# Optimization experiments

Hardware: AMD Instinct MI355X
Metric: run time of the kernel (lower is better)

Reference implementation:

```python
import jax, jax.numpy as jnp
import numpy as np

B, N = 128, 128
FEAT_IN = 6   # feature_dim(4) + class + score
E = 32        # embedding_dim
NUM_CLASSES = 80


def setup_inputs() -> dict:
    key = jax.random.key(0)
    ks = jax.random.split(key, 20)
    def glorot(k, shape):
        fan_in, fan_out = shape[0], shape[1]
        lim = jnp.sqrt(6.0 / (fan_in + fan_out)).astype(jnp.float32)
        return jax.random.uniform(k, shape, jnp.float32, -lim, lim)
    return {
        'boxes': jax.random.uniform(ks[0], (B, N, 4), jnp.float32),
        'classes': jax.random.randint(ks[1], (B, N), 0, NUM_CLASSES),
        'scores': jax.random.uniform(ks[2], (B, N), jnp.float32),
        'num_objects': jax.random.randint(ks[3], (B,), 1, N + 1),
        # feature_encoder: Linear(6->32), ReLU, Linear(32->32)
        'W1': glorot(ks[4], (FEAT_IN, E)), 'b1': jnp.zeros((E,), jnp.float32),
        'W2': glorot(ks[5], (E, E)),       'b2': jnp.zeros((E,), jnp.float32),
        # isObject: Linear(32->32), ReLU, Linear(32->1), Sigmoid
        'Wo1': glorot(ks[6], (E, E)),  'bo1': jnp.zeros((E,), jnp.float32),
        'Wo2': glorot(ks[7], (E, 1)),  'bo2': jnp.zeros((1,), jnp.float32),
        # sameClass: Linear(64->32), ReLU, Linear(32->1), Sigmoid
        'Ws1': glorot(ks[8], (2 * E, E)), 'bs1': jnp.zeros((E,), jnp.float32),
        'Ws2': glorot(ks[9], (E, 1)),     'bs2': jnp.zeros((1,), jnp.float32),
    }


def reference(boxes, classes, scores, num_objects, W1, b1, W2, b2,
              Wo1, bo1, Wo2, bo2, Ws1, bs1, Ws2, bs2):
    # encode: [B,N,6] -> [B,N,E]
    combined = jnp.concatenate(
        [boxes, classes.astype(jnp.float32)[..., None], scores[..., None]], axis=-1)
    enc = jax.nn.relu(combined @ W1 + b1) @ W2 + b2                 # [B,N,E]

    # isObject predicate -> [B,N]
    isobj = jax.nn.sigmoid(jax.nn.relu(enc @ Wo1 + bo1) @ Wo2 + bo2)[..., 0]

    # sameClass on all pairs: split concat-weight so we never build [B,N,N,2E]
    Wsx, Wsy = Ws1[:E], Ws1[E:]
    hx = enc @ Wsx                                                  # [B,N,E]
    hy = enc @ Wsy                                                  # [B,N,E]
    h = jax.nn.relu(hx[:, :, None, :] + hy[:, None, :, :] + bs1)    # [B,N,N,E]
    same = jax.nn.sigmoid(h @ Ws2 + bs2)[..., 0]                    # [B,N,N] (x,y)

    # inner = And_min(isObject(y), sameClass(x,y))
    inner = jnp.minimum(isobj[:, None, :], same)                    # [B,N,N]

    mask = jnp.arange(N)[None, :] < num_objects[:, None]            # [B,N] valid objs
    n = num_objects.astype(jnp.float32)
    denom = jnp.maximum(n, 1.0)

    # Exists_y = mean over valid y
    exists = jnp.sum(inner * mask[:, None, :], axis=-1) / denom[:, None]  # [B,N]

    # outer = Or_max(Not(isObject(x)), exists)
    outer = jnp.maximum(1.0 - isobj, exists)                        # [B,N]

    # Forall_x = min over valid x (pad with 1.0, never the min for valid batches)
    sat_b = jnp.min(jnp.where(mask, outer, 1.0), axis=-1)           # [B]

    valid = (num_objects > 0).astype(jnp.float32)
    cnt = jnp.sum(valid)
    total = jnp.where(cnt > 0,
                      jnp.sum(sat_b * valid) / jnp.maximum(cnt, 1.0),
                      jnp.float32(1.0))
    return total
```

## Files before the change

kernel.cpp:

```cpp
#include <hip/hip_runtime.h>

#define BB 128
#define NN 128
#define EE 32

#define SAT_OFF 0
#define CNT_OFF 128
#define HX_OFF  256
#define HY_OFF  (HX_OFF + 16384 * 32)
#define ISO_OFF (HY_OFF + 16384 * 32)

__global__ __launch_bounds__(256) void encode_kernel(
    const float* __restrict__ boxes, const int* __restrict__ classes,
    const float* __restrict__ scores,
    const float* __restrict__ W1, const float* __restrict__ b1,
    const float* __restrict__ W2, const float* __restrict__ b2,
    const float* __restrict__ Wo1, const float* __restrict__ bo1,
    const float* __restrict__ Wo2, const float* __restrict__ bo2,
    const float* __restrict__ Ws1, float* __restrict__ ws)
{
    __shared__ float sm[4740];

    const int t = threadIdx.x;

    if (blockIdx.x == 0) {
        if (t < 128) ((unsigned*)ws)[SAT_OFF + t] = 0x7F7F7F7Fu;
        if (t == 128) ((unsigned*)ws)[CNT_OFF] = 0u;
    }

    ((float4*)(sm + 224))[t]        = ((const float4*)W2)[t];
    ((float4*)(sm + 1280))[t]       = ((const float4*)Wo1)[t];
    ((float4*)(sm + 2692))[t]       = ((const float4*)Ws1)[t];
    ((float4*)(sm + 2692))[t + 256] = ((const float4*)Ws1)[t + 256];
    if (t < 48) ((float4*)sm)[t] = ((const float4*)W1)[t];
    if (t < 32) {
        sm[192 + t]  = b1[t];
        sm[1248 + t] = b2[t];
        sm[2304 + t] = bo1[t];
        sm[2336 + t] = Wo2[t];
    }
    if (t == 0) sm[2368] = bo2[0];
    __syncthreads();

    const int il = t >> 5;
    const int e  = t & 31;
    const int item = blockIdx.x * 8 + il;

    const float4 bx = ((const float4*)boxes)[item];
    const float c4 = (float)classes[item];
    const float c5 = scores[item];

    float h1 = sm[192 + e];
    h1 = fmaf(bx.x, sm[0 * 32 + e], h1);
    h1 = fmaf(bx.y, sm[1 * 32 + e], h1);
    h1 = fmaf(bx.z, sm[2 * 32 + e], h1);
    h1 = fmaf(bx.w, sm[3 * 32 + e], h1);
    h1 = fmaf(c4,   sm[4 * 32 + e], h1);
    h1 = fmaf(c5,   sm[5 * 32 + e], h1);
    h1 = fmaxf(h1, 0.f);

    float* row = sm + 2372 + il * 40;
    row[e] = h1;

    float a0 = 0.f, a1 = 0.f, a2 = 0.f, a3 = 0.f;
#pragma unroll
    for (int kk = 0; kk < 8; kk++) {
        const float4 h = *(const float4*)(row + kk * 4);
        a0 = fmaf(h.x, sm[224 + (4 * kk + 0) * 32 + e], a0);
        a1 = fmaf(h.y, sm[224 + (4 * kk + 1) * 32 + e], a1);
        a2 = fmaf(h.z, sm[224 + (4 * kk + 2) * 32 + e], a2);
        a3 = fmaf(h.w, sm[224 + (4 * kk + 3) * 32 + e], a3);
    }
    const float enc = ((a0 + a1) + (a2 + a3)) + sm[1248 + e];
    row[e] = enc;

    float u = sm[2304 + e];
    float hx = 0.f, hy = 0.f;
#pragma unroll
    for (int kk = 0; kk < 8; kk++) {
        const float4 ec = *(const float4*)(row + kk * 4);
        const int k0 = 4 * kk;
        u  = fmaf(ec.x, sm[1280 + (k0 + 0) * 32 + e], u);
        u  = fmaf(ec.y, sm[1280 + (k0 + 1) * 32 + e], u);
        u  = fmaf(ec.z, sm[1280 + (k0 + 2) * 32 + e], u);
        u  = fmaf(ec.w, sm[1280 + (k0 + 3) * 32 + e], u);
        hx = fmaf(ec.x, sm[2692 + (k0 + 0) * 32 + e], hx);
        hx = fmaf(ec.y, sm[2692 + (k0 + 1) * 32 + e], hx);
        hx = fmaf(ec.z, sm[2692 + (k0 + 2) * 32 + e], hx);
        hx = fmaf(ec.w, sm[2692 + (k0 + 3) * 32 + e], hx);
        hy = fmaf(ec.x, sm[2692 + (32 + k0 + 0) * 32 + e], hy);
        hy = fmaf(ec.y, sm[2692 + (32 + k0 + 1) * 32 + e], hy);
        hy = fmaf(ec.z, sm[2692 + (32 + k0 + 2) * 32 + e], hy);
        hy = fmaf(ec.w, sm[2692 + (32 + k0 + 3) * 32 + e], hy);
    }
    u = fmaxf(u, 0.f);

    float v = u * sm[2336 + e];
    v += __shfl_xor(v, 16, 32);
    v += __shfl_xor(v, 8, 32);
    v += __shfl_xor(v, 4, 32);
    v += __shfl_xor(v, 2, 32);
    v += __shfl_xor(v, 1, 32);

    ws[HX_OFF + item * 32 + e] = hx;
    ws[HY_OFF + item * 32 + e] = hy;
    if (e == 0)
        ws[ISO_OFF + item] = 1.f / (1.f + __expf(-(v + sm[2368])));
}

__global__ __launch_bounds__(256) void pairs_kernel(
    const float* __restrict__ bs1, const float* __restrict__ Ws2,
    const float* __restrict__ bs2, const int* __restrict__ num_objects,
    float* __restrict__ ws, float* __restrict__ out, int nblocks)
{
    __shared__ float hyS[128 * 36];
    __shared__ float hxS[32 * 36];
    __shared__ float isoS[128];
    __shared__ float wred[4];
    __shared__ int lastFlag;
    __shared__ float r1[4], r2[4];

    const int t = threadIdx.x;
    const int b = blockIdx.x >> 2;
    const int q = blockIdx.x & 3;

    const float4* hyg4 = (const float4*)(ws + HY_OFF + b * 128 * 32);
#pragma unroll
    for (int it = 0; it < 4; it++) {
        const int idx = t + it * 256;
        ((float4*)(hyS + (idx >> 3) * 36))[idx & 7] = hyg4[idx];
    }
    {
        const float4* hxg4 = (const float4*)(ws + HX_OFF + (b * 128 + q * 32) * 32);
        ((float4*)(hxS + (t >> 3) * 36))[t & 7] = hxg4[t];
    }
    if (t < 128) isoS[t] = ws[ISO_OFF + b * 128 + t];
    __syncthreads();

    const int nb = num_objects[b];
    const int il = t >> 3;
    const int i  = q * 32 + il;
    const int s  = t & 7;

    float hxb[32];
#pragma unroll
    for (int kk = 0; kk < 8; kk++) {
        const float4 h = ((const float4*)(hxS + il * 36))[kk];
        hxb[4 * kk + 0] = h.x + bs1[4 * kk + 0];
        hxb[4 * kk + 1] = h.y + bs1[4 * kk + 1];
        hxb[4 * kk + 2] = h.z + bs1[4 * kk + 2];
        hxb[4 * kk + 3] = h.w + bs1[4 * kk + 3];
    }
    float w2[32];
#pragma unroll
    for (int k = 0; k < 32; k++) w2[k] = Ws2[k];
    const float bbias = bs2[0];

    float acc = 0.f;
    for (int j = s; j < nb; j += 8) {
        const float4* hr4 = (const float4*)(hyS + j * 36);
        float d0 = bbias, d1 = 0.f, d2 = 0.f, d3 = 0.f;
#pragma unroll
        for (int kk = 0; kk < 8; kk++) {
            const float4 h = hr4[kk];
            const int k0 = 4 * kk;
            d0 = fmaf(fmaxf(hxb[k0 + 0] + h.x, 0.f), w2[k0 + 0], d0);
            d1 = fmaf(fmaxf(hxb[k0 + 1] + h.y, 0.f), w2[k0 + 1], d1);
            d2 = fmaf(fmaxf(hxb[k0 + 2] + h.z, 0.f), w2[k0 + 2], d2);
            d3 = fmaf(fmaxf(hxb[k0 + 3] + h.w, 0.f), w2[k0 + 3], d3);
        }
        const float d = (d0 + d1) + (d2 + d3);
        const float same = 1.f / (1.f + __expf(-d));
        acc += fminf(isoS[j], same);
    }
    acc += __shfl_xor(acc, 1);
    acc += __shfl_xor(acc, 2);
    acc += __shfl_xor(acc, 4);

    const float exists = acc / (float)(nb > 1 ? nb : 1);
    const float outer = fmaxf(1.f - isoS[i], exists);
    float val = (i < nb) ? outer : 1.f;

    val = fminf(val, __shfl_xor(val, 8));
    val = fminf(val, __shfl_xor(val, 16));
    val = fminf(val, __shfl_xor(val, 32));
    if ((t & 63) == 0) wred[t >> 6] = val;
    __syncthreads();

    if (t == 0) {
        const float m = fminf(fminf(wred[0], wred[1]), fminf(wred[2], wred[3]));
        atomicMin((unsigned*)ws + SAT_OFF + b, __float_as_uint(m));
        __threadfence();
        const unsigned old = __hip_atomic_fetch_add((unsigned*)ws + CNT_OFF, 1u,
                                                    __ATOMIC_ACQ_REL, __HIP_MEMORY_SCOPE_AGENT);
        lastFlag = (old == (unsigned)(nblocks - 1)) ? 1 : 0;
    }
    __syncthreads();

    if (lastFlag) {
        float contrib = 0.f, vcnt = 0.f;
        if (t < 128) {
            const int nbt = num_objects[t];
            const unsigned sbits = __hip_atomic_load((unsigned*)ws + SAT_OFF + t,
                                                     __ATOMIC_RELAXED, __HIP_MEMORY_SCOPE_AGENT);
            const float sat = __uint_as_float(sbits);
            const float valid = (nbt > 0) ? 1.f : 0.f;
            contrib = sat * valid;
            vcnt = valid;
        }
#pragma unroll
        for (int off = 1; off < 64; off <<= 1) {
            contrib += __shfl_xor(contrib, off);
            vcnt += __shfl_xor(vcnt, off);
        }
        if ((t & 63) == 0) { r1[t >> 6] = contrib; r2[t >> 6] = vcnt; }
        __syncthreads();
        if (t == 0) {
            const float sc = r1[0] + r1[1] + r1[2] + r1[3];
            const float cn = r2[0] + r2[1] + r2[2] + r2[3];
            out[0] = (cn > 0.f) ? (sc / cn) : 1.f;
        }
    }
}

extern "C" void kernel_launch(void* const* d_in, const int* in_sizes, int n_in,
                              void* d_out, int out_size, void* d_ws, size_t ws_size,
                              hipStream_t stream)
{
    const float* boxes       = (const float*)d_in[0];
    const int*   classes     = (const int*)d_in[1];
    const float* scores      = (const float*)d_in[2];
    const int*   num_objects = (const int*)d_in[3];
    const float* W1  = (const float*)d_in[4];
    const float* b1  = (const float*)d_in[5];
    const float* W2  = (const float*)d_in[6];
    const float* b2  = (const float*)d_in[7];
    const float* Wo1 = (const float*)d_in[8];
    const float* bo1 = (const float*)d_in[9];
    const float* Wo2 = (const float*)d_in[10];
    const float* bo2 = (const float*)d_in[11];
    const float* Ws1 = (const float*)d_in[12];
    const float* bs1 = (const float*)d_in[13];
    const float* Ws2 = (const float*)d_in[14];
    const float* bs2 = (const float*)d_in[15];

    float* ws  = (float*)d_ws;
    float* out = (float*)d_out;

    encode_kernel<<<2048, 256, 0, stream>>>(boxes, classes, scores,
                                            W1, b1, W2, b2, Wo1, bo1, Wo2, bo2,
                                            Ws1, ws);
    const int nblocks = 128 * 4;
    pairs_kernel<<<nblocks, 256, 0, stream>>>(bs1, Ws2, bs2, num_objects,
                                              ws, out, nblocks);
}
```

Measured before the change: 112.0 us.

## Compute encoder MLP with one thread per object using register arrays

Restructures the encode kernel so each thread processes a whole object, keeping hidden, encoding, hx, hy and u vectors in registers. Weights are read directly from global memory with uniform indices (scalar loads), replacing the shared-memory staging, barrier and warp-shuffle reduction. The launch changes to 256 blocks of 64 threads. Outputs are written as float4 stores per item. The cost is heavy register pressure (about 128+ live floats), possible spills, and far fewer waves in flight to hide latency.

Result: slower. 159.5 us (+42.4%).

```diff
diff --git a/kernel.cpp b/kernel.cpp
--- a/kernel.cpp
+++ b/kernel.cpp
@@ -10,7 +10,7 @@
 #define HY_OFF  (HX_OFF + 16384 * 32)
 #define ISO_OFF (HY_OFF + 16384 * 32)
 
-__global__ __launch_bounds__(256) void encode_kernel(
+__global__ __launch_bounds__(64, 1) void encode_kernel(
     const float* __restrict__ boxes, const int* __restrict__ classes,
     const float* __restrict__ scores,
     const float* __restrict__ W1, const float* __restrict__ b1,
@@ -19,93 +19,70 @@
     const float* __restrict__ Wo2, const float* __restrict__ bo2,
     const float* __restrict__ Ws1, float* __restrict__ ws)
 {
-    __shared__ float sm[4740];
-
     const int t = threadIdx.x;
+    const int item = blockIdx.x * 64 + t;
 
     if (blockIdx.x == 0) {
-        if (t < 128) ((unsigned*)ws)[SAT_OFF + t] = 0x7F7F7F7Fu;
-        if (t == 128) ((unsigned*)ws)[CNT_OFF] = 0u;
-    }
-
-    ((float4*)(sm + 224))[t]        = ((const float4*)W2)[t];
-    ((float4*)(sm + 1280))[t]       = ((const float4*)Wo1)[t];
-    ((float4*)(sm + 2692))[t]       = ((const float4*)Ws1)[t];
-    ((float4*)(sm + 2692))[t + 256] = ((const float4*)Ws1)[t + 256];
-    if (t < 48) ((float4*)sm)[t] = ((const float4*)W1)[t];
-    if (t < 32) {
-        sm[192 + t]  = b1[t];
-        sm[1248 + t] = b2[t];
-        sm[2304 + t] = bo1[t];
-        sm[2336 + t] = Wo2[t];
-    }
-    if (t == 0) sm[2368] = bo2[0];
-    __syncthreads();
-
-    const int il = t >> 5;
-    const int e  = t & 31;
-    const int item = blockIdx.x * 8 + il;
+        ((unsigned*)ws)[SAT_OFF + t]      = 0x7F7F7F7Fu;
+        ((unsigned*)ws)[SAT_OFF + 64 + t] = 0x7F7F7F7Fu;
+        if (t == 0) ((unsigned*)ws)[CNT_OFF] = 0u;
+    }
 
     const float4 bx = ((const float4*)boxes)[item];
     const float c4 = (float)classes[item];
     const float c5 = scores[item];
 
-    float h1 = sm[192 + e];
-    h1 = fmaf(bx.x, sm[0 * 32 + e], h1);
-    h1 = fmaf(bx.y, sm[1 * 32 + e], h1);
-    h1 = fmaf(bx.z, sm[2 * 32 + e], h1);
-    h1 = fmaf(bx.w, sm[3 * 32 + e], h1);
-    h1 = fmaf(c4,   sm[4 * 32 + e], h1);
-    h1 = fmaf(c5,   sm[5 * 32 + e], h1);
-    h1 = fmaxf(h1, 0.f);
-
-    float* row = sm + 2372 + il * 40;
-    row[e] = h1;
-
-    float a0 = 0.f, a1 = 0.f, a2 = 0.f, a3 = 0.f;
+    float h[32];
+#pragma unroll
+    for (int e = 0; e < 32; e++) {
+        float v = b1[e];
+        v = fmaf(bx.x, W1[0 * 32 + e], v);
+        v = fmaf(bx.y, W1[1 * 32 + e], v);
+        v = fmaf(bx.z, W1[2 * 32 + e], v);
+        v = fmaf(bx.w, W1[3 * 32 + e], v);
+        v = fmaf(c4,   W1[4 * 32 + e], v);
+        v = fmaf(c5,   W1[5 * 32 + e], v);
+        h[e] = fmaxf(v, 0.f);
+    }
+
+    float enc[32];
+#pragma unroll
+    for (int e = 0; e < 32; e++) enc[e] = b2[e];
+#pragma unroll
+    for (int k = 0; k < 32; k++) {
+        const float hk = h[k];
+#pragma unroll
+        for (int e = 0; e < 32; e++)
+            enc[e] = fmaf(hk, W2[k * 32 + e], enc[e]);
+    }
+
+    float u[32], hx[32], hy[32];
+#pragma unroll
+    for (int e = 0; e < 32; e++) { u[e] = bo1[e]; hx[e] = 0.f; hy[e] = 0.f; }
+#pragma unroll
+    for (int k = 0; k < 32; k++) {
+        const float ek = enc[k];
+#pragma unroll
+        for (int e = 0; e < 32; e++) {
+            u[e]  = fmaf(ek, Wo1[k * 32 + e], u[e]);
+            hx[e] = fmaf(ek, Ws1[k * 32 + e], hx[e]);
+            hy[e] = fmaf(ek, Ws1[(32 + k) * 32 + e], hy[e]);
+        }
+    }
+
+    float z = bo2[0];
+#pragma unroll
+    for (int e = 0; e < 32; e++)
+        z = fmaf(fmaxf(u[e], 0.f), Wo2[e], z);
+
+    float4* ox = (float4*)(ws + HX_OFF + item * 32);
+    float4* oy = (float4*)(ws + HY_OFF + item * 32);
 #pragma unroll
     for (int kk = 0; kk < 8; kk++) {
-        const float4 h = *(const float4*)(row + kk * 4);
-        a0 = fmaf(h.x, sm[224 + (4 * kk + 0) * 32 + e], a0);
-        a1 = fmaf(h.y, sm[224 + (4 * kk + 1) * 32 + e], a1);
-        a2 = fmaf(h.z, sm[224 + (4 * kk + 2) * 32 + e], a2);
-        a3 = fmaf(h.w, sm[224 + (4 * kk + 3) * 32 + e], a3);
-    }
-    const float enc = ((a0 + a1) + (a2 + a3)) + sm[1248 + e];
-    row[e] = enc;
-
-    float u = sm[2304 + e];
-    float hx = 0.f, hy = 0.f;
-#pragma unroll
-    for (int kk = 0; kk < 8; kk++) {
-        const float4 ec = *(const float4*)(row + kk * 4);
-        const int k0 = 4 * kk;
-        u  = fmaf(ec.x, sm[1280 + (k0 + 0) * 32 + e], u);
-        u  = fmaf(ec.y, sm[1280 + (k0 + 1) * 32 + e], u);
-        u  = fmaf(ec.z, sm[1280 + (k0 + 2) * 32 + e], u);
-        u  = fmaf(ec.w, sm[1280 + (k0 + 3) * 32 + e], u);
-        hx = fmaf(ec.x, sm[2692 + (k0 + 0) * 32 + e], hx);
-        hx = fmaf(ec.y, sm[2692 + (k0 + 1) * 32 + e], hx);
-        hx = fmaf(ec.z, sm[2692 + (k0 + 2) * 32 + e], hx);
-        hx = fmaf(ec.w, sm[2692 + (k0 + 3) * 32 + e], hx);
-        hy = fmaf(ec.x, sm[2692 + (32 + k0 + 0) * 32 + e], hy);
-        hy = fmaf(ec.y, sm[2692 + (32 + k0 + 1) * 32 + e], hy);
-        hy = fmaf(ec.z, sm[2692 + (32 + k0 + 2) * 32 + e], hy);
-        hy = fmaf(ec.w, sm[2692 + (32 + k0 + 3) * 32 + e], hy);
-    }
-    u = fmaxf(u, 0.f);
-
-    float v = u * sm[2336 + e];
-    v += __shfl_xor(v, 16, 32);
-    v += __shfl_xor(v, 8, 32);
-    v += __shfl_xor(v, 4, 32);
-    v += __shfl_xor(v, 2, 32);
-    v += __shfl_xor(v, 1, 32);
-
-    ws[HX_OFF + item * 32 + e] = hx;
-    ws[HY_OFF + item * 32 + e] = hy;
-    if (e == 0)
-        ws[ISO_OFF + item] = 1.f / (1.f + __expf(-(v + sm[2368])));
+        ox[kk] = make_float4(hx[4 * kk], hx[4 * kk + 1], hx[4 * kk + 2], hx[4 * kk + 3]);
+        oy[kk] = make_float4(hy[4 * kk], hy[4 * kk + 1], hy[4 * kk + 2], hy[4 * kk + 3]);
+    }
+    ws[ISO_OFF + item] = 1.f / (1.f + __expf(-z));
 }
 
 __global__ __launch_bounds__(256) void pairs_kernel(
@@ -247,9 +224,9 @@
     float* ws  = (float*)d_ws;
     float* out = (float*)d_out;
 
-    encode_kernel<<<2048, 256, 0, stream>>>(boxes, classes, scores,
-                                            W1, b1, W2, b2, Wo1, bo1, Wo2, bo2,
-                                            Ws1, ws);
+    encode_kernel<<<256, 64, 0, stream>>>(boxes, classes, scores,
+                                          W1, b1, W2, b2, Wo1, bo1, Wo2, bo2,
+                                          Ws1, ws);
     const int nblocks = 128 * 4;
     pairs_kernel<<<nblocks, 256, 0, stream>>>(bs1, Ws2, bs2, num_objects,
                                               ws, out, nblocks);
```

## Keep encoder weights in registers and double per-thread work in pairs kernel

Applied to the files above, without the earlier changes.

The encode kernel no longer stages all weights into shared memory. Each thread instead keeps its weight column in registers and processes four items per warp-group, with a quarter as many blocks, so weight loads are amortized. The pairs kernel has each thread handle two x rows against each loaded hy row, which halves the block count and the hy reloads from shared memory per pair. The cost is much higher register pressure (over 130 floats in encode, 64+ in pairs), which can lower occupancy, and fewer blocks means less parallelism on a large GPU.

Measured after the change: 102.4 us. 1.09x faster.

```diff
diff --git a/kernel.cpp b/kernel.cpp
--- a/kernel.cpp
+++ b/kernel.cpp
@@ -19,93 +19,100 @@
     const float* __restrict__ Wo2, const float* __restrict__ bo2,
     const float* __restrict__ Ws1, float* __restrict__ ws)
 {
-    __shared__ float sm[4740];
+    __shared__ float rows[8 * 36];
 
     const int t = threadIdx.x;
+    const int e = t & 31;
+    const int g = t >> 5;
 
     if (blockIdx.x == 0) {
         if (t < 128) ((unsigned*)ws)[SAT_OFF + t] = 0x7F7F7F7Fu;
         if (t == 128) ((unsigned*)ws)[CNT_OFF] = 0u;
     }
 
-    ((float4*)(sm + 224))[t]        = ((const float4*)W2)[t];
-    ((float4*)(sm + 1280))[t]       = ((const float4*)Wo1)[t];
-    ((float4*)(sm + 2692))[t]       = ((const float4*)Ws1)[t];
-    ((float4*)(sm + 2692))[t + 256] = ((const float4*)Ws1)[t + 256];
-    if (t < 48) ((float4*)sm)[t] = ((const float4*)W1)[t];
-    if (t < 32) {
-        sm[192 + t]  = b1[t];
-        sm[1248 + t] = b2[t];
-        sm[2304 + t] = bo1[t];
-        sm[2336 + t] = Wo2[t];
-    }
-    if (t == 0) sm[2368] = bo2[0];
-    __syncthreads();
-
-    const int il = t >> 5;
-    const int e  = t & 31;
-    const int item = blockIdx.x * 8 + il;
-
-    const float4 bx = ((const float4*)boxes)[item];
-    const float c4 = (float)classes[item];
-    const float c5 = scores[item];
-
-    float h1 = sm[192 + e];
-    h1 = fmaf(bx.x, sm[0 * 32 + e], h1);
-    h1 = fmaf(bx.y, sm[1 * 32 + e], h1);
-    h1 = fmaf(bx.z, sm[2 * 32 + e], h1);
-    h1 = fmaf(bx.w, sm[3 * 32 + e], h1);
-    h1 = fmaf(c4,   sm[4 * 32 + e], h1);
-    h1 = fmaf(c5,   sm[5 * 32 + e], h1);
-    h1 = fmaxf(h1, 0.f);
-
-    float* row = sm + 2372 + il * 40;
-    row[e] = h1;
-
-    float a0 = 0.f, a1 = 0.f, a2 = 0.f, a3 = 0.f;
-#pragma unroll
-    for (int kk = 0; kk < 8; kk++) {
-        const float4 h = *(const float4*)(row + kk * 4);
-        a0 = fmaf(h.x, sm[224 + (4 * kk + 0) * 32 + e], a0);
-        a1 = fmaf(h.y, sm[224 + (4 * kk + 1) * 32 + e], a1);
-        a2 = fmaf(h.z, sm[224 + (4 * kk + 2) * 32 + e], a2);
-        a3 = fmaf(h.w, sm[224 + (4 * kk + 3) * 32 + e], a3);
-    }
-    const float enc = ((a0 + a1) + (a2 + a3)) + sm[1248 + e];
-    row[e] = enc;
-
-    float u = sm[2304 + e];
-    float hx = 0.f, hy = 0.f;
-#pragma unroll
-    for (int kk = 0; kk < 8; kk++) {
-        const float4 ec = *(const float4*)(row + kk * 4);
-        const int k0 = 4 * kk;
-        u  = fmaf(ec.x, sm[1280 + (k0 + 0) * 32 + e], u);
-        u  = fmaf(ec.y, sm[1280 + (k0 + 1) * 32 + e], u);
-        u  = fmaf(ec.z, sm[1280 + (k0 + 2) * 32 + e], u);
-        u  = fmaf(ec.w, sm[1280 + (k0 + 3) * 32 + e], u);
-        hx = fmaf(ec.x, sm[2692 + (k0 + 0) * 32 + e], hx);
-        hx = fmaf(ec.y, sm[2692 + (k0 + 1) * 32 + e], hx);
-        hx = fmaf(ec.z, sm[2692 + (k0 + 2) * 32 + e], hx);
-        hx = fmaf(ec.w, sm[2692 + (k0 + 3) * 32 + e], hx);
-        hy = fmaf(ec.x, sm[2692 + (32 + k0 + 0) * 32 + e], hy);
-        hy = fmaf(ec.y, sm[2692 + (32 + k0 + 1) * 32 + e], hy);
-        hy = fmaf(ec.z, sm[2692 + (32 + k0 + 2) * 32 + e], hy);
-        hy = fmaf(ec.w, sm[2692 + (32 + k0 + 3) * 32 + e], hy);
-    }
-    u = fmaxf(u, 0.f);
-
-    float v = u * sm[2336 + e];
-    v += __shfl_xor(v, 16, 32);
-    v += __shfl_xor(v, 8, 32);
-    v += __shfl_xor(v, 4, 32);
-    v += __shfl_xor(v, 2, 32);
-    v += __shfl_xor(v, 1, 32);
-
-    ws[HX_OFF + item * 32 + e] = hx;
-    ws[HY_OFF + item * 32 + e] = hy;
-    if (e == 0)
-        ws[ISO_OFF + item] = 1.f / (1.f + __expf(-(v + sm[2368])));
+    float w1c[6];
+#pragma unroll
+    for (int f = 0; f < 6; f++) w1c[f] = W1[f * 32 + e];
+    float w2c[32], wo1c[32], wsxc[32], wsyc[32];
+#pragma unroll
+    for (int k = 0; k < 32; k++) {
+        w2c[k]  = W2[k * 32 + e];
+        wo1c[k] = Wo1[k * 32 + e];
+        wsxc[k] = Ws1[k * 32 + e];
+        wsyc[k] = Ws1[(32 + k) * 32 + e];
+    }
+    const float b1e  = b1[e];
+    const float b2e  = b2[e];
+    const float bo1e = bo1[e];
+    const float wo2e = Wo2[e];
+    const float bo2s = bo2[0];
+
+    float* row = rows + g * 36;
+    const int itemBase = blockIdx.x * 32 + g * 4;
+
+#pragma unroll 1
+    for (int it = 0; it < 4; ++it) {
+        const int item = itemBase + it;
+
+        const float4 bx = ((const float4*)boxes)[item];
+        const float c4 = (float)classes[item];
+        const float c5 = scores[item];
+
+        float h1 = b1e;
+        h1 = fmaf(bx.x, w1c[0], h1);
+        h1 = fmaf(bx.y, w1c[1], h1);
+        h1 = fmaf(bx.z, w1c[2], h1);
+        h1 = fmaf(bx.w, w1c[3], h1);
+        h1 = fmaf(c4,   w1c[4], h1);
+        h1 = fmaf(c5,   w1c[5], h1);
+        h1 = fmaxf(h1, 0.f);
+
+        row[e] = h1;
+
+        float a0 = 0.f, a1 = 0.f, a2 = 0.f, a3 = 0.f;
+#pragma unroll
+        for (int kk = 0; kk < 8; kk++) {
+            const float4 h = *(const float4*)(row + kk * 4);
+            a0 = fmaf(h.x, w2c[4 * kk + 0], a0);
+            a1 = fmaf(h.y, w2c[4 * kk + 1], a1);
+            a2 = fmaf(h.z, w2c[4 * kk + 2], a2);
+            a3 = fmaf(h.w, w2c[4 * kk + 3], a3);
+        }
+        const float enc = ((a0 + a1) + (a2 + a3)) + b2e;
+        row[e] = enc;
+
+        float u = bo1e, hx = 0.f, hy = 0.f;
+#pragma unroll
+        for (int kk = 0; kk < 8; kk++) {
+            const float4 ec = *(const float4*)(row + kk * 4);
+            const int k0 = 4 * kk;
+            u  = fmaf(ec.x, wo1c[k0 + 0], u);
+            u  = fmaf(ec.y, wo1c[k0 + 1], u);
+            u  = fmaf(ec.z, wo1c[k0 + 2], u);
+            u  = fmaf(ec.w, wo1c[k0 + 3], u);
+            hx = fmaf(ec.x, wsxc[k0 + 0], hx);
+            hx = fmaf(ec.y, wsxc[k0 + 1], hx);
+            hx = fmaf(ec.z, wsxc[k0 + 2], hx);
+            hx = fmaf(ec.w, wsxc[k0 + 3], hx);
+            hy = fmaf(ec.x, wsyc[k0 + 0], hy);
+            hy = fmaf(ec.y, wsyc[k0 + 1], hy);
+            hy = fmaf(ec.z, wsyc[k0 + 2], hy);
+            hy = fmaf(ec.w, wsyc[k0 + 3], hy);
+        }
+        u = fmaxf(u, 0.f);
+
+        float v = u * wo2e;
+        v += __shfl_xor(v, 16, 32);
+        v += __shfl_xor(v, 8, 32);
+        v += __shfl_xor(v, 4, 32);
+        v += __shfl_xor(v, 2, 32);
+        v += __shfl_xor(v, 1, 32);
+
+        ws[HX_OFF + item * 32 + e] = hx;
+        ws[HY_OFF + item * 32 + e] = hy;
+        if (e == 0)
+            ws[ISO_OFF + item] = 1.f / (1.f + __expf(-(v + bo2s)));
+    }
 }
 
 __global__ __launch_bounds__(256) void pairs_kernel(
@@ -114,15 +121,15 @@
     float* __restrict__ ws, float* __restrict__ out, int nblocks)
 {
     __shared__ float hyS[128 * 36];
-    __shared__ float hxS[32 * 36];
+    __shared__ float hxS[64 * 36];
     __shared__ float isoS[128];
     __shared__ float wred[4];
     __shared__ int lastFlag;
     __shared__ float r1[4], r2[4];
 
     const int t = threadIdx.x;
-    const int b = blockIdx.x >> 2;
-    const int q = blockIdx.x & 3;
+    const int b = blockIdx.x >> 1;
+    const int half = blockIdx.x & 1;
 
     const float4* hyg4 = (const float4*)(ws + HY_OFF + b * 128 * 32);
 #pragma unroll
@@ -130,56 +137,73 @@
         const int idx = t + it * 256;
         ((float4*)(hyS + (idx >> 3) * 36))[idx & 7] = hyg4[idx];
     }
-    {
-        const float4* hxg4 = (const float4*)(ws + HX_OFF + (b * 128 + q * 32) * 32);
-        ((float4*)(hxS + (t >> 3) * 36))[t & 7] = hxg4[t];
+    const float4* hxg4 = (const float4*)(ws + HX_OFF + (b * 128 + half * 64) * 32);
+#pragma unroll
+    for (int it = 0; it < 2; it++) {
+        const int idx = t + it * 256;
+        ((float4*)(hxS + (idx >> 3) * 36))[idx & 7] = hxg4[idx];
     }
     if (t < 128) isoS[t] = ws[ISO_OFF + b * 128 + t];
     __syncthreads();
 
     const int nb = num_objects[b];
-    const int il = t >> 3;
-    const int i  = q * 32 + il;
+    const int p  = t >> 3;
+    const int i0 = half * 64 + p * 2;
+    const int i1 = i0 + 1;
     const int s  = t & 7;
 
-    float hxb[32];
+    float hxb0[32], hxb1[32];
 #pragma unroll
     for (int kk = 0; kk < 8; kk++) {
-        const float4 h = ((const float4*)(hxS + il * 36))[kk];
-        hxb[4 * kk + 0] = h.x + bs1[4 * kk + 0];
-        hxb[4 * kk + 1] = h.y + bs1[4 * kk + 1];
-        hxb[4 * kk + 2] = h.z + bs1[4 * kk + 2];
-        hxb[4 * kk + 3] = h.w + bs1[4 * kk + 3];
+        const float4 a = ((const float4*)(hxS + (p * 2) * 36))[kk];
+        const float4 c = ((const float4*)(hxS + (p * 2 + 1) * 36))[kk];
+        const int k0 = 4 * kk;
+        hxb0[k0 + 0] = a.x + bs1[k0 + 0];  hxb1[k0 + 0] = c.x + bs1[k0 + 0];
+        hxb0[k0 + 1] = a.y + bs1[k0 + 1];  hxb1[k0 + 1] = c.y + bs1[k0 + 1];
+        hxb0[k0 + 2] = a.z + bs1[k0 + 2];  hxb1[k0 + 2] = c.z + bs1[k0 + 2];
+        hxb0[k0 + 3] = a.w + bs1[k0 + 3];  hxb1[k0 + 3] = c.w + bs1[k0 + 3];
     }
     float w2[32];
 #pragma unroll
     for (int k = 0; k < 32; k++) w2[k] = Ws2[k];
     const float bbias = bs2[0];
 
-    float acc = 0.f;
+    float acc0 = 0.f, acc1 = 0.f;
     for (int j = s; j < nb; j += 8) {
         const float4* hr4 = (const float4*)(hyS + j * 36);
         float d0 = bbias, d1 = 0.f, d2 = 0.f, d3 = 0.f;
+        float e0 = bbias, e1 = 0.f, e2 = 0.f, e3 = 0.f;
 #pragma unroll
         for (int kk = 0; kk < 8; kk++) {
             const float4 h = hr4[kk];
             const int k0 = 4 * kk;
-            d0 = fmaf(fmaxf(hxb[k0 + 0] + h.x, 0.f), w2[k0 + 0], d0);
-            d1 = fmaf(fmaxf(hxb[k0 + 1] + h.y, 0.f), w2[k0 + 1], d1);
-            d2 = fmaf(fmaxf(hxb[k0 + 2] + h.z, 0.f), w2[k0 + 2], d2);
-            d3 = fmaf(fmaxf(hxb[k0 + 3] + h.w, 0.f), w2[k0 + 3], d3);
-        }
-        const float d = (d0 + d1) + (d2 + d3);
-        const float same = 1.f / (1.f + __expf(-d));
-        acc += fminf(isoS[j], same);
-    }
-    acc += __shfl_xor(acc, 1);
-    acc += __shfl_xor(acc, 2);
-    acc += __shfl_xor(acc, 4);
-
-    const float exists = acc / (float)(nb > 1 ? nb : 1);
-    const float outer = fmaxf(1.f - isoS[i], exists);
-    float val = (i < nb) ? outer : 1.f;
+            d0 = fmaf(fmaxf(hxb0[k0 + 0] + h.x, 0.f), w2[k0 + 0], d0);
+            d1 = fmaf(fmaxf(hxb0[k0 + 1] + h.y, 0.f), w2[k0 + 1], d1);
+            d2 = fmaf(fmaxf(hxb0[k0 + 2] + h.z, 0.f), w2[k0 + 2], d2);
+            d3 = fmaf(fmaxf(hxb0[k0 + 3] + h.w, 0.f), w2[k0 + 3], d3);
+            e0 = fmaf(fmaxf(hxb1[k0 + 0] + h.x, 0.f), w2[k0 + 0], e0);
+            e1 = fmaf(fmaxf(hxb1[k0 + 1] + h.y, 0.f), w2[k0 + 1], e1);
+            e2 = fmaf(fmaxf(hxb1[k0 + 2] + h.z, 0.f), w2[k0 + 2], e2);
+            e3 = fmaf(fmaxf(hxb1[k0 + 3] + h.w, 0.f), w2[k0 + 3], e3);
+        }
+        const float dd = (d0 + d1) + (d2 + d3);
+        const float ee = (e0 + e1) + (e2 + e3);
+        const float same0 = 1.f / (1.f + __expf(-dd));
+        const float same1 = 1.f / (1.f + __expf(-ee));
+        const float iso_j = isoS[j];
+        acc0 += fminf(iso_j, same0);
+        acc1 += fminf(iso_j, same1);
+    }
+    acc0 += __shfl_xor(acc0, 1);  acc1 += __shfl_xor(acc1, 1);
+    acc0 += __shfl_xor(acc0, 2);  acc1 += __shfl_xor(acc1, 2);
+    acc0 += __shfl_xor(acc0, 4);  acc1 += __shfl_xor(acc1, 4);
+
+    const float denom = (float)(nb > 1 ? nb : 1);
+    const float ex0 = acc0 / denom;
+    const float ex1 = acc1 / denom;
+    const float o0 = fmaxf(1.f - isoS[i0], ex0);
+    const float o1 = fmaxf(1.f - isoS[i1], ex1);
+    float val = fminf((i0 < nb) ? o0 : 1.f, (i1 < nb) ? o1 : 1.f);
 
     val = fminf(val, __shfl_xor(val, 8));
     val = fminf(val, __shfl_xor(val, 16));
@@ -247,10 +271,10 @@
     float* ws  = (float*)d_ws;
     float* out = (float*)d_out;
 
-    encode_kernel<<<2048, 256, 0, stream>>>(boxes, classes, scores,
-                                            W1, b1, W2, b2, Wo1, bo1, Wo2, bo2,
-                                            Ws1, ws);
-    const int nblocks = 128 * 4;
+    encode_kernel<<<512, 256, 0, stream>>>(boxes, classes, scores,
+                                           W1, b1, W2, b2, Wo1, bo1, Wo2, bo2,
+                                           Ws1, ws);
+    const int nblocks = 128 * 2;
     pairs_kernel<<<nblocks, 256, 0, stream>>>(bs1, Ws2, bs2, num_objects,
                                               ws, out, nblocks);
 }
```
